# Optimization experiments

Measured on AMD Instinct MI355X. Metric: run time of the kernel, lower is better.

Reference implementation:

```python
import jax, jax.numpy as jnp
import numpy as np
import math

B, S, D_MODEL, N_HEAD = 4, 2048, 1024, 16
D_K = D_MODEL // N_HEAD
ROPE_THETA = 10000.0


def _rope(x):
    # x: [B, H, S, Dk]; interleaved-pair rotary embedding.
    b, h, s, d = x.shape
    inv_freq = ROPE_THETA ** (-jnp.arange(0, d, 2, dtype=jnp.float32) / d)  # [d/2]
    ang = jnp.arange(s, dtype=jnp.float32)[:, None] * inv_freq[None, :]      # [S, d/2]
    cos, sin = jnp.cos(ang), jnp.sin(ang)
    x1, x2 = x[..., 0::2], x[..., 1::2]
    r1 = x1 * cos - x2 * sin
    r2 = x1 * sin + x2 * cos
    return jnp.stack([r1, r2], axis=-1).reshape(b, h, s, d)


def setup_inputs() -> dict:
    key = jax.random.key(0)
    ks = jax.random.split(key, 7)
    sc = 1.0 / math.sqrt(D_MODEL)
    return {
        "q": jax.random.normal(ks[0], (B, S, D_MODEL), jnp.float32),
        "k": jax.random.normal(ks[1], (B, S, D_MODEL), jnp.float32),
        "v": jax.random.normal(ks[2], (B, S, D_MODEL), jnp.float32),
        "Wq": jax.random.normal(ks[3], (D_MODEL, D_MODEL), jnp.float32) * sc,
        "Wk": jax.random.normal(ks[4], (D_MODEL, D_MODEL), jnp.float32) * sc,
        "Wv": jax.random.normal(ks[5], (D_MODEL, D_MODEL), jnp.float32) * sc,
        "Wo": jax.random.normal(ks[6], (D_MODEL, D_MODEL), jnp.float32) * sc,
    }


def _split(x):
    b, s, d = x.shape
    return x.reshape(b, s, N_HEAD, d // N_HEAD).transpose(0, 2, 1, 3)  # [B,H,S,Dk]


def reference(q, k, v, Wq, Wk, Wv, Wo):
    q = jnp.einsum("bsd,de->bse", q, Wq)
    k = jnp.einsum("bsd,de->bse", k, Wk)
    v = jnp.einsum("bsd,de->bse", v, Wv)
    qh, kh, vh = _split(q), _split(k), _split(v)
    qh, kh = _rope(qh), _rope(kh)
    scale = 1.0 / math.sqrt(D_K)
    score = jnp.einsum("bhqd,bhkd->bhqk", qh, kh) * scale  # [B,H,S,S]
    attn = jax.nn.softmax(score, axis=-1)
    out = jnp.einsum("bhqk,bhkd->bhqd", attn, vh)
    out = out.transpose(0, 2, 1, 3).reshape(q.shape[0], q.shape[1], D_MODEL)
    return jnp.einsum("bsd,de->bse", out, Wo)
```

## Files before the change

kernel.cpp:

```cpp
#include <hip/hip_runtime.h>
#include <stdint.h>

#define Bv 4
#define Sv 2048
#define Dv 1024
#define Hv 16
#define DKv 64
#define BSv (Bv * Sv)

typedef unsigned short u16;
typedef __attribute__((ext_vector_type(8))) short short8;
typedef __attribute__((ext_vector_type(8))) unsigned short u16x8;
typedef __attribute__((ext_vector_type(4))) unsigned short u16x4;
typedef __attribute__((ext_vector_type(4))) float f32x4;
typedef __attribute__((ext_vector_type(16))) float f32x16;

__device__ __forceinline__ u16 f2bf(float f) {
  union { float f; uint32_t u; } x; x.f = f;
  uint32_t r = x.u + 0x7FFFu + ((x.u >> 16) & 1u);
  return (u16)(r >> 16);
}

__device__ __forceinline__ void gl_lds16(const void* g, void* l) {
  __builtin_amdgcn_global_load_lds(
      (__attribute__((address_space(1))) void*)g,
      (__attribute__((address_space(3))) void*)l, 16, 0, 0);
}

__device__ __forceinline__ f32x4 mfma16(short8 a, short8 b, f32x4 c) {
  return __builtin_amdgcn_mfma_f32_16x16x32_bf16(a, b, c, 0, 0, 0);
}
__device__ __forceinline__ f32x16 mfma32(short8 a, short8 b, f32x16 c) {
  return __builtin_amdgcn_mfma_f32_32x32x16_bf16(a, b, c, 0, 0, 0);
}

__global__ __launch_bounds__(256) void conv_qkv(
    const float* __restrict__ q, const float* __restrict__ k,
    const float* __restrict__ v, u16* __restrict__ qb, u16* __restrict__ kb,
    u16* __restrict__ vb) {
  const float* src = (blockIdx.y == 0) ? q : (blockIdx.y == 1 ? k : v);
  u16* dst = (blockIdx.y == 0) ? qb : (blockIdx.y == 1 ? kb : vb);
  int i = (blockIdx.x * 256 + threadIdx.x) * 8;
  const float4* s4 = (const float4*)(src + i);
  float4 a = s4[0], b = s4[1];
  u16x8 o = { f2bf(a.x), f2bf(a.y), f2bf(a.z), f2bf(a.w),
              f2bf(b.x), f2bf(b.y), f2bf(b.z), f2bf(b.w) };
  *(u16x8*)(dst + i) = o;
}

__global__ __launch_bounds__(256) void conv_wt(
    const float* __restrict__ w0, const float* __restrict__ w1,
    const float* __restrict__ w2, const float* __restrict__ w3,
    u16* __restrict__ t0, u16* __restrict__ t1, u16* __restrict__ t2,
    u16* __restrict__ t3) {
  const float* W = (blockIdx.z == 0) ? w0 : (blockIdx.z == 1 ? w1 : (blockIdx.z == 2 ? w2 : w3));
  u16* T = (blockIdx.z == 0) ? t0 : (blockIdx.z == 1 ? t1 : (blockIdx.z == 2 ? t2 : t3));
  __shared__ u16 tile[64][72];
  int nb = blockIdx.x * 64, kb = blockIdx.y * 64;
  int t = threadIdx.x;
#pragma unroll
  for (int p = 0; p < 4; ++p) {
    int idx = p * 256 + t;
    int r = idx >> 4;
    int c4 = (idx & 15) * 4;
    float4 vv = *(const float4*)(W + (size_t)(kb + r) * Dv + nb + c4);
    tile[c4 + 0][r] = f2bf(vv.x);
    tile[c4 + 1][r] = f2bf(vv.y);
    tile[c4 + 2][r] = f2bf(vv.z);
    tile[c4 + 3][r] = f2bf(vv.w);
  }
  __syncthreads();
#pragma unroll
  for (int p = 0; p < 4; ++p) {
    int idx = p * 256 + t;
    int r = idx >> 4;
    int c4 = (idx & 15) * 4;
    u16x4 o = { tile[r][c4], tile[r][c4 + 1], tile[r][c4 + 2], tile[r][c4 + 3] };
    *(u16x4*)(T + (size_t)(nb + r) * Dv + kb + c4) = o;
  }
}

__global__ __launch_bounds__(256) void gemm_bt(
    const u16* __restrict__ A0, const u16* __restrict__ A1, const u16* __restrict__ A2,
    const u16* __restrict__ B0, const u16* __restrict__ B1, const u16* __restrict__ B2,
    void* __restrict__ O0, void* __restrict__ O1, void* __restrict__ O2,
    int modeSel) {
  __shared__ u16 As[2][128 * 64];
  __shared__ u16 Bs[2][128 * 64];
  int z = blockIdx.z;
  const u16* A  = (z == 0) ? A0 : (z == 1 ? A1 : A2);
  const u16* Bt = (z == 0) ? B0 : (z == 1 ? B1 : B2);
  void* Out     = (z == 0) ? O0 : (z == 1 ? O1 : O2);
  int mode = (modeSel < 0) ? z : modeSel;

  int tid = threadIdx.x;
  int lane = tid & 63, wid = tid >> 6;
  int quad = lane >> 4, cc = lane & 15;
  int wm = (wid >> 1) * 64, wn = (wid & 1) * 64;
  int m0 = blockIdx.x * 128, n0 = blockIdx.y * 128;

  f32x4 acc[4][4];
#pragma unroll
  for (int mi = 0; mi < 4; ++mi)
#pragma unroll
    for (int ni = 0; ni < 4; ++ni) {
      f32x4 zf = {0.f, 0.f, 0.f, 0.f};
      acc[mi][ni] = zf;
    }

#pragma unroll
  for (int p = 0; p < 4; ++p) {
    int slot = p * 256 + tid;
    int row = slot >> 3, cl = slot & 7;
    int cg = cl ^ (row & 7);
    gl_lds16(A + (size_t)(m0 + row) * Dv + cg * 8, &As[0][slot * 8]);
    gl_lds16(Bt + (size_t)(n0 + row) * Dv + cg * 8, &Bs[0][slot * 8]);
  }

  for (int ki = 0; ki < Dv / 64; ++ki) {
    int cur = ki & 1;
    __syncthreads();

    if (ki + 1 < Dv / 64) {
      int k1 = (ki + 1) * 64;
#pragma unroll
      for (int p = 0; p < 4; ++p) {
        int slot = p * 256 + tid;
        int row = slot >> 3, cl = slot & 7;
        int cg = cl ^ (row & 7);
        gl_lds16(A + (size_t)(m0 + row) * Dv + k1 + cg * 8, &As[1 - cur][slot * 8]);
        gl_lds16(Bt + (size_t)(n0 + row) * Dv + k1 + cg * 8, &Bs[1 - cur][slot * 8]);
      }
    }

#pragma unroll
    for (int kk = 0; kk < 2; ++kk) {
      short8 af[4], bf[4];
#pragma unroll
      for (int mi = 0; mi < 4; ++mi) {
        int row = wm + mi * 16 + cc;
        int cg = kk * 4 + quad;
        af[mi] = *(const short8*)&As[cur][row * 64 + (cg ^ (row & 7)) * 8];
      }
#pragma unroll
      for (int ni = 0; ni < 4; ++ni) {
        int row = wn + ni * 16 + cc;
        int cg = kk * 4 + quad;
        bf[ni] = *(const short8*)&Bs[cur][row * 64 + (cg ^ (row & 7)) * 8];
      }
#pragma unroll
      for (int mi = 0; mi < 4; ++mi)
#pragma unroll
        for (int ni = 0; ni < 4; ++ni)
          acc[mi][ni] = mfma16(af[mi], bf[ni], acc[mi][ni]);
    }
  }

  if (mode <= 1) {
    u16* O = (u16*)Out;
    float postscale = (mode == 0) ? 0.18033688011112042f : 1.0f;
#pragma unroll
    for (int ni = 0; ni < 4; ++ni) {
      int n = n0 + wn + ni * 16 + cc;
      int h = n >> 6, d = n & 63;
      float inv = __expf(-(float)(d & 62) * (9.210340372f / 64.0f));
      float sign = (d & 1) ? 1.0f : -1.0f;
#pragma unroll
      for (int mi = 0; mi < 4; ++mi) {
        int mB = m0 + wm + mi * 16 + quad * 4;
#pragma unroll
        for (int r = 0; r < 4; ++r) {
          int m = mB + r;
          int b = m >> 11, s = m & (Sv - 1);
          float val = acc[mi][ni][r];
          float part = __shfl_xor(val, 1);
          float sn, cs;
          __sincosf((float)s * inv, &sn, &cs);
          float outv = (val * cs + sign * part * sn) * postscale;
          O[((size_t)(b * Hv + h) * Sv + s) * DKv + d] = f2bf(outv);
        }
      }
    }
  } else if (mode == 2) {
    u16* O = (u16*)Out;
#pragma unroll
    for (int ni = 0; ni < 4; ++ni) {
      int n = n0 + wn + ni * 16 + cc;
      int h = n >> 6, d = n & 63;
#pragma unroll
      for (int mi = 0; mi < 4; ++mi) {
        int mB = m0 + wm + mi * 16 + quad * 4;
        int b = mB >> 11, s = mB & (Sv - 1);
        u16x4 o4 = { f2bf(acc[mi][ni][0]), f2bf(acc[mi][ni][1]),
                     f2bf(acc[mi][ni][2]), f2bf(acc[mi][ni][3]) };
        *(u16x4*)&O[((size_t)(b * Hv + h) * DKv + d) * Sv + s] = o4;
      }
    }
  } else {
    float* O = (float*)Out;
#pragma unroll
    for (int ni = 0; ni < 4; ++ni) {
      int n = n0 + wn + ni * 16 + cc;
#pragma unroll
      for (int mi = 0; mi < 4; ++mi) {
        int mB = m0 + wm + mi * 16 + quad * 4;
#pragma unroll
        for (int r = 0; r < 4; ++r)
          O[(size_t)(mB + r) * Dv + n] = acc[mi][ni][r];
      }
    }
  }
}

__global__ __launch_bounds__(256, 2) void attn(
    const u16* __restrict__ Qp, const u16* __restrict__ Kp,
    const u16* __restrict__ Vt, u16* __restrict__ ctx) {
  __shared__ u16 Ks[2][64 * 64];
  __shared__ u16 Vs[2][64 * 64];
  int tid = threadIdx.x;
  int lane = tid & 63, wid = tid >> 6;
  int hi = lane >> 5, c32 = lane & 31;
  int sz = (c32 & 7) ^ ((c32 >> 3) & 3);
  int bh = blockIdx.y;
  int q0 = blockIdx.x * 256 + wid * 64;
  const u16* Qh = Qp + (size_t)bh * Sv * DKv;
  const u16* Kh = Kp + (size_t)bh * Sv * DKv;
  const u16* Vh = Vt + (size_t)bh * Sv * DKv;

  const short8 ones = { (short)0x3F80, (short)0x3F80, (short)0x3F80, (short)0x3F80,
                        (short)0x3F80, (short)0x3F80, (short)0x3F80, (short)0x3F80 };

  short8 qf[2][4];
#pragma unroll
  for (int qs = 0; qs < 2; ++qs)
#pragma unroll
    for (int dk = 0; dk < 4; ++dk)
      qf[qs][dk] = *(const short8*)&Qh[(size_t)(q0 + qs * 32 + c32) * DKv + dk * 16 + hi * 8];

  f32x16 o[2][2];
  f32x16 ol[2];
#pragma unroll
  for (int qs = 0; qs < 2; ++qs) {
#pragma unroll
    for (int dt = 0; dt < 2; ++dt)
#pragma unroll
      for (int r = 0; r < 16; ++r) o[qs][dt][r] = 0.f;
#pragma unroll
    for (int r = 0; r < 16; ++r) ol[qs][r] = 0.f;
  }

#pragma unroll
  for (int p = 0; p < 2; ++p) {
    int slot = p * 256 + tid;
    int row = slot >> 3, cl = slot & 7;
    int cg = cl ^ ((row & 7) ^ ((row >> 3) & 3));
    gl_lds16(Kh + (size_t)row * DKv + cg * 8, &Ks[0][slot * 8]);
    gl_lds16(Vh + (size_t)row * Sv + cg * 8, &Vs[0][slot * 8]);
  }

  for (int kt = 0; kt < Sv / 64; ++kt) {
    int cur = kt & 1;
    __syncthreads();

    if (kt + 1 < Sv / 64) {
      int s1 = (kt + 1) * 64;
#pragma unroll
      for (int p = 0; p < 2; ++p) {
        int slot = p * 256 + tid;
        int row = slot >> 3, cl = slot & 7;
        int cg = cl ^ ((row & 7) ^ ((row >> 3) & 3));
        gl_lds16(Kh + (size_t)(s1 + row) * DKv + cg * 8, &Ks[1 - cur][slot * 8]);
        gl_lds16(Vh + (size_t)row * Sv + s1 + cg * 8, &Vs[1 - cur][slot * 8]);
      }
    }

#pragma unroll
    for (int half = 0; half < 2; ++half) {
      short8 kf[4];
#pragma unroll
      for (int dk = 0; dk < 4; ++dk)
        kf[dk] = *(const short8*)&Ks[cur][(half * 32 + c32) * 64 + (((dk * 2 + hi) ^ sz)) * 8];

      f32x16 st[2];
#pragma unroll
      for (int qs = 0; qs < 2; ++qs) {
#pragma unroll
        for (int r = 0; r < 16; ++r) st[qs][r] = 0.f;
#pragma unroll
        for (int dk = 0; dk < 4; ++dk)
          st[qs] = mfma32(kf[dk], qf[qs][dk], st[qs]);
      }

#pragma unroll
      for (int pp = 0; pp < 2; ++pp) {
        int pk = half * 2 + pp;
        short8 vf[2];
#pragma unroll
        for (int dt = 0; dt < 2; ++dt)
          vf[dt] = *(const short8*)&Vs[cur][(dt * 32 + c32) * 64 + (((pk * 2 + hi) ^ sz)) * 8];
#pragma unroll
        for (int qs = 0; qs < 2; ++qs) {
          float e0 = __builtin_amdgcn_exp2f(st[qs][8 * pp + 0]);
          float e1 = __builtin_amdgcn_exp2f(st[qs][8 * pp + 1]);
          float e2 = __builtin_amdgcn_exp2f(st[qs][8 * pp + 2]);
          float e3 = __builtin_amdgcn_exp2f(st[qs][8 * pp + 3]);
          float e4 = __builtin_amdgcn_exp2f(st[qs][8 * pp + 4]);
          float e5 = __builtin_amdgcn_exp2f(st[qs][8 * pp + 5]);
          float e6 = __builtin_amdgcn_exp2f(st[qs][8 * pp + 6]);
          float e7 = __builtin_amdgcn_exp2f(st[qs][8 * pp + 7]);
          uint32_t plo0 = __builtin_amdgcn_perm(__float_as_uint(e1), __float_as_uint(e0), 0x07060302u);
          uint32_t plo1 = __builtin_amdgcn_perm(__float_as_uint(e3), __float_as_uint(e2), 0x07060302u);
          uint32_t phi0 = __builtin_amdgcn_perm(__float_as_uint(e5), __float_as_uint(e4), 0x07060302u);
          uint32_t phi1 = __builtin_amdgcn_perm(__float_as_uint(e7), __float_as_uint(e6), 0x07060302u);
          uint32_t s0 = hi ? plo0 : phi0;
          uint32_t s1 = hi ? plo1 : phi1;
          uint32_t r0 = (uint32_t)__shfl_xor((int)s0, 32);
          uint32_t r1 = (uint32_t)__shfl_xor((int)s1, 32);
          union { uint32_t u[4]; short8 s8; } pu;
          pu.u[0] = hi ? r0 : plo0;
          pu.u[1] = hi ? r1 : plo1;
          pu.u[2] = hi ? phi0 : r0;
          pu.u[3] = hi ? phi1 : r1;
          ol[qs] = mfma32(pu.s8, ones, ol[qs]);
          o[qs][0] = mfma32(pu.s8, vf[0], o[qs][0]);
          o[qs][1] = mfma32(pu.s8, vf[1], o[qs][1]);
        }
      }
    }
  }

  int b = bh >> 4, h = bh & 15;
#pragma unroll
  for (int qs = 0; qs < 2; ++qs)
#pragma unroll
    for (int r = 0; r < 16; ++r) {
      int q = q0 + qs * 32 + (r & 3) + 8 * (r >> 2) + 4 * hi;
      float linv = 1.0f / ol[qs][r];
#pragma unroll
      for (int dt = 0; dt < 2; ++dt) {
        int d = h * DKv + dt * 32 + c32;
        ctx[((size_t)b * Sv + q) * Dv + d] = f2bf(o[qs][dt][r] * linv);
      }
    }
}

extern "C" void kernel_launch(void* const* d_in, const int* in_sizes, int n_in,
                              void* d_out, int out_size, void* d_ws, size_t ws_size,
                              hipStream_t stream) {
  (void)in_sizes; (void)n_in; (void)out_size; (void)ws_size;
  const float* q  = (const float*)d_in[0];
  const float* k  = (const float*)d_in[1];
  const float* v  = (const float*)d_in[2];
  const float* Wq = (const float*)d_in[3];
  const float* Wk = (const float*)d_in[4];
  const float* Wv = (const float*)d_in[5];
  const float* Wo = (const float*)d_in[6];

  char* ws = (char*)d_ws;
  size_t off = 0;
  const size_t big = (size_t)BSv * Dv * sizeof(u16);
  const size_t wsz = (size_t)Dv * Dv * sizeof(u16);
  u16* qb  = (u16*)(ws + off); off += big;
  u16* kb  = (u16*)(ws + off); off += big;
  u16* vb  = (u16*)(ws + off); off += big;
  u16* Wqt = (u16*)(ws + off); off += wsz;
  u16* Wkt = (u16*)(ws + off); off += wsz;
  u16* Wvt = (u16*)(ws + off); off += wsz;
  u16* Wot = (u16*)(ws + off); off += wsz;
  u16* Qp  = (u16*)(ws + off); off += big;
  u16* Kp  = (u16*)(ws + off); off += big;
  u16* Vtr = (u16*)(ws + off); off += big;
  u16* ctx = (u16*)(ws + off); off += big;

  conv_qkv<<<dim3(BSv * Dv / (256 * 8), 3), 256, 0, stream>>>(q, k, v, qb, kb, vb);
  conv_wt<<<dim3(Dv / 64, Dv / 64, 4), 256, 0, stream>>>(Wq, Wk, Wv, Wo, Wqt, Wkt, Wvt, Wot);
  gemm_bt<<<dim3(BSv / 128, Dv / 128, 3), 256, 0, stream>>>(
      qb, kb, vb, Wqt, Wkt, Wvt, Qp, Kp, Vtr, -1);
  attn<<<dim3(Sv / 256, Bv * Hv), 256, 0, stream>>>(Qp, Kp, Vtr, ctx);
  gemm_bt<<<dim3(BSv / 128, Dv / 128, 1), 256, 0, stream>>>(
      ctx, ctx, ctx, Wot, Wot, Wot, d_out, d_out, d_out, 3);
}
```

Before: 335.5 us.

## Triple-buffer GEMM and attention loads with vmcnt waits, enlarge GEMM tile, swizzle blocks

Both the projection GEMM and the attention kernel move from double to triple-buffered LDS staging. Each iteration now waits with an explicit s_waitcnt vmcnt followed by a raw barrier, so prefetches issued two tiles ahead can stay in flight across the sync. The GEMM block becomes 512 threads computing a 128x256 tile, and both kernels remap block indices so neighbouring blocks that share operands run together for better L2 reuse. The costs are more LDS per block, which may limit occupancy, and reliance on hand-counted vmcnt values being correct.

```diff
diff --git a/kernel.cpp b/kernel.cpp
--- a/kernel.cpp
+++ b/kernel.cpp
@@ -32,6 +32,13 @@
 }
 __device__ __forceinline__ f32x16 mfma32(short8 a, short8 b, f32x16 c) {
   return __builtin_amdgcn_mfma_f32_32x32x16_bf16(a, b, c, 0, 0, 0);
+}
+
+template <int N>
+__device__ __forceinline__ void tile_sync() {
+  asm volatile("s_waitcnt vmcnt(%0)" ::"n"(N) : "memory");
+  __builtin_amdgcn_s_barrier();
+  asm volatile("" ::: "memory");
 }
 
 __global__ __launch_bounds__(256) void conv_qkv(
@@ -80,13 +87,13 @@
   }
 }
 
-__global__ __launch_bounds__(256) void gemm_bt(
+__global__ __launch_bounds__(512, 2) void gemm_bt(
     const u16* __restrict__ A0, const u16* __restrict__ A1, const u16* __restrict__ A2,
     const u16* __restrict__ B0, const u16* __restrict__ B1, const u16* __restrict__ B2,
     void* __restrict__ O0, void* __restrict__ O1, void* __restrict__ O2,
     int modeSel) {
-  __shared__ u16 As[2][128 * 64];
-  __shared__ u16 Bs[2][128 * 64];
+  __shared__ u16 As[3][128 * 64];
+  __shared__ u16 Bs[3][256 * 64];
   int z = blockIdx.z;
   const u16* A  = (z == 0) ? A0 : (z == 1 ? A1 : A2);
   const u16* Bt = (z == 0) ? B0 : (z == 1 ? B1 : B2);
@@ -96,8 +103,10 @@
   int tid = threadIdx.x;
   int lane = tid & 63, wid = tid >> 6;
   int quad = lane >> 4, cc = lane & 15;
-  int wm = (wid >> 1) * 64, wn = (wid & 1) * 64;
-  int m0 = blockIdx.x * 128, n0 = blockIdx.y * 128;
+  int wm = (wid >> 2) * 64, wn = (wid & 3) * 64;
+  int bx = blockIdx.x;
+  int swz = (bx & 7) * 32 + (bx >> 3);
+  int m0 = (swz >> 2) * 128, n0 = (swz & 3) * 256;
 
   f32x4 acc[4][4];
 #pragma unroll
@@ -108,34 +117,37 @@
       acc[mi][ni] = zf;
     }
 
-#pragma unroll
-  for (int p = 0; p < 4; ++p) {
-    int slot = p * 256 + tid;
-    int row = slot >> 3, cl = slot & 7;
-    int cg = cl ^ (row & 7);
-    gl_lds16(A + (size_t)(m0 + row) * Dv + cg * 8, &As[0][slot * 8]);
-    gl_lds16(Bt + (size_t)(n0 + row) * Dv + cg * 8, &Bs[0][slot * 8]);
-  }
-
-  for (int ki = 0; ki < Dv / 64; ++ki) {
-    int cur = ki & 1;
-    __syncthreads();
-
-    if (ki + 1 < Dv / 64) {
-      int k1 = (ki + 1) * 64;
-#pragma unroll
-      for (int p = 0; p < 4; ++p) {
-        int slot = p * 256 + tid;
-        int row = slot >> 3, cl = slot & 7;
-        int cg = cl ^ (row & 7);
-        gl_lds16(A + (size_t)(m0 + row) * Dv + k1 + cg * 8, &As[1 - cur][slot * 8]);
-        gl_lds16(Bt + (size_t)(n0 + row) * Dv + k1 + cg * 8, &Bs[1 - cur][slot * 8]);
-      }
-    }
+  auto stage = [&](int ki, int b) {
+    int k0 = ki * 64;
+#pragma unroll
+    for (int p = 0; p < 2; ++p) {
+      int slot = p * 512 + tid;
+      int row = slot >> 3, cl = slot & 7;
+      int cg = cl ^ (row & 7);
+      gl_lds16(A + (size_t)(m0 + row) * Dv + k0 + cg * 8, &As[b][slot * 8]);
+    }
+#pragma unroll
+    for (int p = 0; p < 4; ++p) {
+      int slot = p * 512 + tid;
+      int row = slot >> 3, cl = slot & 7;
+      int cg = cl ^ (row & 7);
+      gl_lds16(Bt + (size_t)(n0 + row) * Dv + k0 + cg * 8, &Bs[b][slot * 8]);
+    }
+  };
+
+  stage(0, 0);
+  stage(1, 1);
+
+  const int NT = Dv / 64;
+  int cur = 0, nxt = 2;
+#pragma unroll 1
+  for (int t = 0; t < NT; ++t) {
+    if (t + 1 < NT) tile_sync<6>(); else tile_sync<0>();
+    if (t + 2 < NT) stage(t + 2, nxt);
 
 #pragma unroll
     for (int kk = 0; kk < 2; ++kk) {
-      short8 af[4], bf[4];
+      short8 af[4], bfr[4];
 #pragma unroll
       for (int mi = 0; mi < 4; ++mi) {
         int row = wm + mi * 16 + cc;
@@ -146,14 +158,16 @@
       for (int ni = 0; ni < 4; ++ni) {
         int row = wn + ni * 16 + cc;
         int cg = kk * 4 + quad;
-        bf[ni] = *(const short8*)&Bs[cur][row * 64 + (cg ^ (row & 7)) * 8];
+        bfr[ni] = *(const short8*)&Bs[cur][row * 64 + (cg ^ (row & 7)) * 8];
       }
 #pragma unroll
       for (int mi = 0; mi < 4; ++mi)
 #pragma unroll
         for (int ni = 0; ni < 4; ++ni)
-          acc[mi][ni] = mfma16(af[mi], bf[ni], acc[mi][ni]);
-    }
+          acc[mi][ni] = mfma16(af[mi], bfr[ni], acc[mi][ni]);
+    }
+    cur = (cur == 2) ? 0 : cur + 1;
+    nxt = (nxt == 2) ? 0 : nxt + 1;
   }
 
   if (mode <= 1) {
@@ -212,17 +226,19 @@
   }
 }
 
-__global__ __launch_bounds__(256, 2) void attn(
+__global__ __launch_bounds__(256, 3) void attn(
     const u16* __restrict__ Qp, const u16* __restrict__ Kp,
     const u16* __restrict__ Vt, u16* __restrict__ ctx) {
-  __shared__ u16 Ks[2][64 * 64];
-  __shared__ u16 Vs[2][64 * 64];
+  __shared__ u16 Ks[3][64 * 64];
+  __shared__ u16 Vs[3][64 * 64];
   int tid = threadIdx.x;
   int lane = tid & 63, wid = tid >> 6;
   int hi = lane >> 5, c32 = lane & 31;
   int sz = (c32 & 7) ^ ((c32 >> 3) & 3);
-  int bh = blockIdx.y;
-  int q0 = blockIdx.x * 256 + wid * 64;
+  int bx = blockIdx.x;
+  int bswz = (bx & 7) * 64 + (bx >> 3);
+  int bh = bswz >> 3;
+  int q0 = (bswz & 7) * 256 + wid * 64;
   const u16* Qh = Qp + (size_t)bh * Sv * DKv;
   const u16* Kh = Kp + (size_t)bh * Sv * DKv;
   const u16* Vh = Vt + (size_t)bh * Sv * DKv;
@@ -249,30 +265,27 @@
     for (int r = 0; r < 16; ++r) ol[qs][r] = 0.f;
   }
 
-#pragma unroll
-  for (int p = 0; p < 2; ++p) {
-    int slot = p * 256 + tid;
-    int row = slot >> 3, cl = slot & 7;
-    int cg = cl ^ ((row & 7) ^ ((row >> 3) & 3));
-    gl_lds16(Kh + (size_t)row * DKv + cg * 8, &Ks[0][slot * 8]);
-    gl_lds16(Vh + (size_t)row * Sv + cg * 8, &Vs[0][slot * 8]);
-  }
-
-  for (int kt = 0; kt < Sv / 64; ++kt) {
-    int cur = kt & 1;
-    __syncthreads();
-
-    if (kt + 1 < Sv / 64) {
-      int s1 = (kt + 1) * 64;
-#pragma unroll
-      for (int p = 0; p < 2; ++p) {
-        int slot = p * 256 + tid;
-        int row = slot >> 3, cl = slot & 7;
-        int cg = cl ^ ((row & 7) ^ ((row >> 3) & 3));
-        gl_lds16(Kh + (size_t)(s1 + row) * DKv + cg * 8, &Ks[1 - cur][slot * 8]);
-        gl_lds16(Vh + (size_t)row * Sv + s1 + cg * 8, &Vs[1 - cur][slot * 8]);
-      }
-    }
+  auto stage = [&](int kt, int b) {
+    int s1 = kt * 64;
+#pragma unroll
+    for (int p = 0; p < 2; ++p) {
+      int slot = p * 256 + tid;
+      int row = slot >> 3, cl = slot & 7;
+      int cg = cl ^ ((row & 7) ^ ((row >> 3) & 3));
+      gl_lds16(Kh + (size_t)(s1 + row) * DKv + cg * 8, &Ks[b][slot * 8]);
+      gl_lds16(Vh + (size_t)row * Sv + s1 + cg * 8, &Vs[b][slot * 8]);
+    }
+  };
+
+  stage(0, 0);
+  stage(1, 1);
+
+  const int NT = Sv / 64;
+  int cur = 0, nxt = 2;
+#pragma unroll 1
+  for (int kt = 0; kt < NT; ++kt) {
+    if (kt + 1 < NT) tile_sync<4>(); else tile_sync<0>();
+    if (kt + 2 < NT) stage(kt + 2, nxt);
 
 #pragma unroll
     for (int half = 0; half < 2; ++half) {
@@ -327,6 +340,8 @@
         }
       }
     }
+    cur = (cur == 2) ? 0 : cur + 1;
+    nxt = (nxt == 2) ? 0 : nxt + 1;
   }
 
   int b = bh >> 4, h = bh & 15;
@@ -374,9 +389,9 @@
 
   conv_qkv<<<dim3(BSv * Dv / (256 * 8), 3), 256, 0, stream>>>(q, k, v, qb, kb, vb);
   conv_wt<<<dim3(Dv / 64, Dv / 64, 4), 256, 0, stream>>>(Wq, Wk, Wv, Wo, Wqt, Wkt, Wvt, Wot);
-  gemm_bt<<<dim3(BSv / 128, Dv / 128, 3), 256, 0, stream>>>(
+  gemm_bt<<<dim3((BSv / 128) * (Dv / 256), 1, 3), 512, 0, stream>>>(
       qb, kb, vb, Wqt, Wkt, Wvt, Qp, Kp, Vtr, -1);
-  attn<<<dim3(Sv / 256, Bv * Hv), 256, 0, stream>>>(Qp, Kp, Vtr, ctx);
-  gemm_bt<<<dim3(BSv / 128, Dv / 128, 1), 256, 0, stream>>>(
+  attn<<<dim3((Sv / 256) * Bv * Hv), 256, 0, stream>>>(Qp, Kp, Vtr, ctx);
+  gemm_bt<<<dim3((BSv / 128) * (Dv / 256), 1, 1), 512, 0, stream>>>(
       ctx, ctx, ctx, Wot, Wot, Wot, d_out, d_out, d_out, 3);
 }
```

Result: slower. 395.3 us (+17.8%).

## Triple-buffer GEMM with 256x128 tiles, 512 threads and swizzled block order

Applied to the files above, without the earlier changes.

The projection GEMM moves from a 128x128 tile with 256 threads and a double buffer to a 256x128 tile with 8 waves and a three-stage LDS ring. Loads run two tiles ahead, synchronised with explicit vmcnt waits and raw barriers, and s_setprio raises wave priority around the MFMA blocks. Blocks are remapped through a swizzle so neighbouring blocks share A/B tiles in cache. This should hide global latency and improve reuse, at the cost of more LDS (144KB per block) and fragile hand-written wait counts.

```diff
diff --git a/kernel.cpp b/kernel.cpp
--- a/kernel.cpp
+++ b/kernel.cpp
@@ -32,6 +32,16 @@
 }
 __device__ __forceinline__ f32x16 mfma32(short8 a, short8 b, f32x16 c) {
   return __builtin_amdgcn_mfma_f32_32x32x16_bf16(a, b, c, 0, 0, 0);
+}
+
+template <int N>
+__device__ __forceinline__ void vwait() {
+  asm volatile("s_waitcnt vmcnt(%0)" ::"n"(N) : "memory");
+}
+__device__ __forceinline__ void bar() {
+  asm volatile("" ::: "memory");
+  __builtin_amdgcn_s_barrier();
+  asm volatile("" ::: "memory");
 }
 
 __global__ __launch_bounds__(256) void conv_qkv(
@@ -80,13 +90,13 @@
   }
 }
 
-__global__ __launch_bounds__(256) void gemm_bt(
+__global__ __launch_bounds__(512, 2) void gemm_bt(
     const u16* __restrict__ A0, const u16* __restrict__ A1, const u16* __restrict__ A2,
     const u16* __restrict__ B0, const u16* __restrict__ B1, const u16* __restrict__ B2,
     void* __restrict__ O0, void* __restrict__ O1, void* __restrict__ O2,
     int modeSel) {
-  __shared__ u16 As[2][128 * 64];
-  __shared__ u16 Bs[2][128 * 64];
+  __shared__ u16 As[3][256 * 64];
+  __shared__ u16 Bs[3][128 * 64];
   int z = blockIdx.z;
   const u16* A  = (z == 0) ? A0 : (z == 1 ? A1 : A2);
   const u16* Bt = (z == 0) ? B0 : (z == 1 ? B1 : B2);
@@ -97,7 +107,9 @@
   int lane = tid & 63, wid = tid >> 6;
   int quad = lane >> 4, cc = lane & 15;
   int wm = (wid >> 1) * 64, wn = (wid & 1) * 64;
-  int m0 = blockIdx.x * 128, n0 = blockIdx.y * 128;
+  int bx = blockIdx.x;
+  int swz = (bx & 7) * 32 + (bx >> 3);
+  int m0 = (swz >> 3) * 256, n0 = (swz & 7) * 128;
 
   f32x4 acc[4][4];
 #pragma unroll
@@ -108,52 +120,68 @@
       acc[mi][ni] = zf;
     }
 
-#pragma unroll
-  for (int p = 0; p < 4; ++p) {
-    int slot = p * 256 + tid;
+  auto stageA2 = [&](int ki, int b, int p0) {
+#pragma unroll
+    for (int p = 0; p < 2; ++p) {
+      int slot = (p0 + p) * 512 + tid;
+      int row = slot >> 3, cl = slot & 7;
+      int cg = cl ^ (row & 7);
+      gl_lds16(A + (size_t)(m0 + row) * Dv + ki * 64 + cg * 8, &As[b][slot * 8]);
+    }
+  };
+  auto stageB1 = [&](int ki, int b, int p0) {
+    int slot = p0 * 512 + tid;
     int row = slot >> 3, cl = slot & 7;
     int cg = cl ^ (row & 7);
-    gl_lds16(A + (size_t)(m0 + row) * Dv + cg * 8, &As[0][slot * 8]);
-    gl_lds16(Bt + (size_t)(n0 + row) * Dv + cg * 8, &Bs[0][slot * 8]);
-  }
-
-  for (int ki = 0; ki < Dv / 64; ++ki) {
-    int cur = ki & 1;
-    __syncthreads();
-
-    if (ki + 1 < Dv / 64) {
-      int k1 = (ki + 1) * 64;
-#pragma unroll
-      for (int p = 0; p < 4; ++p) {
-        int slot = p * 256 + tid;
-        int row = slot >> 3, cl = slot & 7;
-        int cg = cl ^ (row & 7);
-        gl_lds16(A + (size_t)(m0 + row) * Dv + k1 + cg * 8, &As[1 - cur][slot * 8]);
-        gl_lds16(Bt + (size_t)(n0 + row) * Dv + k1 + cg * 8, &Bs[1 - cur][slot * 8]);
-      }
-    }
-
+    gl_lds16(Bt + (size_t)(n0 + row) * Dv + ki * 64 + cg * 8, &Bs[b][slot * 8]);
+  };
+
+  stageA2(0, 0, 0); stageA2(0, 0, 2); stageB1(0, 0, 0); stageB1(0, 0, 1);
+  stageA2(1, 1, 0); stageA2(1, 1, 2); stageB1(1, 1, 0); stageB1(1, 1, 1);
+  vwait<6>();
+  bar();
+
+  const int NT = Dv / 64;
+  int cur = 0, nxt = 2;
+#pragma unroll 1
+  for (int t = 0; t < NT; ++t) {
+    const u16* Ac = &As[cur][0];
+    const u16* Bc = &Bs[cur][0];
 #pragma unroll
     for (int kk = 0; kk < 2; ++kk) {
-      short8 af[4], bf[4];
+      short8 af[4], bfr[4];
 #pragma unroll
       for (int mi = 0; mi < 4; ++mi) {
         int row = wm + mi * 16 + cc;
         int cg = kk * 4 + quad;
-        af[mi] = *(const short8*)&As[cur][row * 64 + (cg ^ (row & 7)) * 8];
+        af[mi] = *(const short8*)&Ac[row * 64 + (cg ^ (row & 7)) * 8];
       }
 #pragma unroll
       for (int ni = 0; ni < 4; ++ni) {
         int row = wn + ni * 16 + cc;
         int cg = kk * 4 + quad;
-        bf[ni] = *(const short8*)&Bs[cur][row * 64 + (cg ^ (row & 7)) * 8];
-      }
+        bfr[ni] = *(const short8*)&Bc[row * 64 + (cg ^ (row & 7)) * 8];
+      }
+      if (t + 2 < NT) {
+        if (kk == 0) { stageA2(t + 2, nxt, 0); stageB1(t + 2, nxt, 0); }
+        else         { stageA2(t + 2, nxt, 2); stageB1(t + 2, nxt, 1); }
+      }
+      bar();
+      __builtin_amdgcn_s_setprio(1);
 #pragma unroll
       for (int mi = 0; mi < 4; ++mi)
 #pragma unroll
         for (int ni = 0; ni < 4; ++ni)
-          acc[mi][ni] = mfma16(af[mi], bf[ni], acc[mi][ni]);
-    }
+          acc[mi][ni] = mfma16(af[mi], bfr[ni], acc[mi][ni]);
+      __builtin_amdgcn_s_setprio(0);
+      if (kk == 0) bar();
+    }
+    if (t < NT - 1) {
+      if (t + 2 < NT) vwait<6>(); else vwait<0>();
+      bar();
+    }
+    cur = (cur == 2) ? 0 : cur + 1;
+    nxt = (nxt == 2) ? 0 : nxt + 1;
   }
 
   if (mode <= 1) {
@@ -374,9 +402,9 @@
 
   conv_qkv<<<dim3(BSv * Dv / (256 * 8), 3), 256, 0, stream>>>(q, k, v, qb, kb, vb);
   conv_wt<<<dim3(Dv / 64, Dv / 64, 4), 256, 0, stream>>>(Wq, Wk, Wv, Wo, Wqt, Wkt, Wvt, Wot);
-  gemm_bt<<<dim3(BSv / 128, Dv / 128, 3), 256, 0, stream>>>(
+  gemm_bt<<<dim3(256, 1, 3), 512, 0, stream>>>(
       qb, kb, vb, Wqt, Wkt, Wvt, Qp, Kp, Vtr, -1);
   attn<<<dim3(Sv / 256, Bv * Hv), 256, 0, stream>>>(Qp, Kp, Vtr, ctx);
-  gemm_bt<<<dim3(BSv / 128, Dv / 128, 1), 256, 0, stream>>>(
+  gemm_bt<<<dim3(256, 1, 1), 512, 0, stream>>>(
       ctx, ctx, ctx, Wot, Wot, Wot, d_out, d_out, d_out, 3);
 }
```

After: 327.7 us. -2.3%, faster.
